# Kernel tuning notes

Measured on AMD Instinct MI355X. Metric: run time of the kernel, lower is better.

Reference implementation:

```python
import jax, jax.numpy as jnp
import numpy as np
from jax import lax

B = 256
INPUT_DIM = 65536
SEQ = 128
VOCAB = INPUT_DIM // SEQ  # 512
LATENT = 128
HIDS = (1024, 512, 256)   # encoder hidden dims (hidden_dims[:-1])
ENC_OUT = 128             # hidden_dims[-1]
GRU_H = 128               # decoder hidden_dim = hidden_dims[-1]
BN_EPS = 1e-5
LRELU_SLOPE = 0.01


def setup_inputs() -> dict:
    key = jax.random.key(0)
    ks = iter(jax.random.split(key, 40))
    def w(shape, scale=0.02):
        return (jax.random.normal(next(ks), shape, dtype=jnp.float32) * scale)
    d = {}
    d['x'] = jax.random.normal(next(ks), (B, INPUT_DIM), dtype=jnp.float32)
    d['eps'] = jax.random.normal(next(ks), (B, LATENT), dtype=jnp.float32)
    dims = (INPUT_DIM,) + HIDS
    # encoder Linear+BN stacks
    for i in range(3):
        d[f'W{i}'] = w((dims[i + 1], dims[i]))
        d[f'b{i}'] = w((dims[i + 1],))
        d[f'g{i}'] = jnp.ones((dims[i + 1],), jnp.float32)
        d[f'be{i}'] = jnp.zeros((dims[i + 1],), jnp.float32)
    d['Wout'] = w((ENC_OUT, HIDS[-1]))
    d['bout'] = w((ENC_OUT,))
    d['Wmu'] = w((LATENT, ENC_OUT)); d['bmu'] = w((LATENT,))
    d['Wlv'] = w((LATENT, ENC_OUT)); d['blv'] = w((LATENT,))
    # GRU (num_layers=1), PyTorch gate order r,z,n
    d['Wih'] = w((3 * GRU_H, LATENT)); d['bih'] = w((3 * GRU_H,))
    d['Whh'] = w((3 * GRU_H, GRU_H)); d['bhh'] = w((3 * GRU_H,))
    d['Wfc'] = w((VOCAB, GRU_H)); d['bfc'] = w((VOCAB,))
    return d


def _bn(h, g, b):
    m = jnp.mean(h, axis=0)
    v = jnp.var(h, axis=0)
    return (h - m) * lax.rsqrt(v + BN_EPS) * g + b


def _lrelu(h):
    return jnp.where(h > 0, h, LRELU_SLOPE * h)


def reference(x, eps, W0, b0, g0, be0, W1, b1, g1, be1, W2, b2, g2, be2,
              Wout, bout, Wmu, bmu, Wlv, blv, Wih, bih, Whh, bhh, Wfc, bfc):
    # ---- encode ----
    h = x
    for W, b, g, be in ((W0, b0, g0, be0), (W1, b1, g1, be1), (W2, b2, g2, be2)):
        h = _lrelu(_bn(h @ W.T + b, g, be))
    h = h @ Wout.T + bout
    h1 = jax.nn.relu(h)
    mu = h1 @ Wmu.T + bmu
    logvar = h1 @ Wlv.T + blv
    # ---- reparameterize ----
    z = mu + eps * jnp.exp(0.5 * logvar)
    # ---- greedy decode: GRU step + argmax + one-hot, seq_length times ----
    # GRU input is the constant z each step -> precompute input projection once
    xp = z @ Wih.T + bih                       # [B, 3H]
    xr, xz, xn = jnp.split(xp, 3, axis=1)
    h0 = jnp.zeros((x.shape[0], GRU_H), x.dtype)

    def step(hid, _):
        hp = hid @ Whh.T + bhh
        hr, hz, hn = jnp.split(hp, 3, axis=1)
        r = jax.nn.sigmoid(xr + hr)
        zg = jax.nn.sigmoid(xz + hz)
        n = jnp.tanh(xn + r * hn)
        h2 = (1.0 - zg) * n + zg * hid
        logits = h2 @ Wfc.T + bfc              # [B, V]
        oh = jax.nn.one_hot(jnp.argmax(logits, axis=1), VOCAB, dtype=logits.dtype)
        return h2, oh

    _, outs = lax.scan(step, h0, None, length=SEQ)  # [S, B, V]
    out = jnp.transpose(outs, (1, 0, 2))            # [B, S, V]
    return out, mu, logvar
```

## Files before the change

kernel.cpp:

```cpp
#include <hip/hip_runtime.h>

#define DI __device__ __forceinline__

typedef __attribute__((ext_vector_type(8))) short s16x8;
typedef __attribute__((ext_vector_type(4))) float f32x4;

DI f32x4 mfma16(s16x8 a, s16x8 b, f32x4 c) {
  return __builtin_amdgcn_mfma_f32_16x16x32_bf16(a, b, c, 0, 0, 0);
}

DI unsigned short f2bf(float f) {
  unsigned int u = __builtin_bit_cast(unsigned int, f);
  u += 0x7fffu + ((u >> 16) & 1u);
  return (unsigned short)(u >> 16);
}
DI float bf2f(unsigned short h) {
  unsigned int u = ((unsigned int)h) << 16;
  return __builtin_bit_cast(float, u);
}
DI void split2(float f, unsigned short &hi, unsigned short &lo) {
  hi = f2bf(f);
  lo = f2bf(f - bf2f(hi));
}

DI unsigned int cvtpk(float a, float b) {
  unsigned int r;
  asm("v_cvt_pk_bf16_f32 %0, %1, %2" : "=v"(r) : "v"(a), "v"(b));
  return r;
}
DI float fromlo(unsigned int u) { return __builtin_bit_cast(float, u << 16); }
DI float fromhi(unsigned int u) { return __builtin_bit_cast(float, u & 0xffff0000u); }

DI void write_pair8(unsigned short* hp, unsigned short* lp, float4 a, float4 b) {
  unsigned int h01 = cvtpk(a.x, a.y), h23 = cvtpk(a.z, a.w);
  unsigned int h45 = cvtpk(b.x, b.y), h67 = cvtpk(b.z, b.w);
  unsigned int l01 = cvtpk(a.x - fromlo(h01), a.y - fromhi(h01));
  unsigned int l23 = cvtpk(a.z - fromlo(h23), a.w - fromhi(h23));
  unsigned int l45 = cvtpk(b.x - fromlo(h45), b.y - fromhi(h45));
  unsigned int l67 = cvtpk(b.z - fromlo(h67), b.w - fromhi(h67));
  uint4 H4; H4.x = h01; H4.y = h23; H4.z = h45; H4.w = h67;
  uint4 L4; L4.x = l01; L4.y = l23; L4.z = l45; L4.w = l67;
  *(uint4*)hp = H4;
  *(uint4*)lp = L4;
}

DI float fsig(float x)  { return __builtin_amdgcn_rcpf(1.f + __expf(-x)); }
DI float ftanhf(float x){ return 1.f - 2.f * __builtin_amdgcn_rcpf(1.f + __expf(2.f * x)); }

template<int M, int N, int K, int KS, bool SWZ>
__global__ __launch_bounds__(256, 2) void k_gemm(const float* __restrict__ A,
                                                 const float* __restrict__ Bw,
                                                 float* __restrict__ P) {
  constexpr int MT = M / 128, NT = N / 128;
  constexpr int KC = K / KS;
  constexpr int ITERS = KC / 32;
  int bid = blockIdx.x;
  int kidx, mt, nt;
  if (SWZ) {
    int xcd = bid & 7, s = bid >> 3;
    kidx = xcd + 8 * (s >> 4);
    int mn = s & 15; mt = mn >> 3; nt = mn & 7;
  } else {
    kidx = bid / (MT * NT);
    int mn = bid % (MT * NT);
    mt = mn / NT; nt = mn % NT;
  }
  int tid = threadIdx.x;
  int w = tid >> 6, lane = tid & 63, q = lane >> 4, l15 = lane & 15;
  int wm = w >> 1, wn = w & 1;

  __shared__ unsigned short Ah[2][4][128][8], Al[2][4][128][8];
  __shared__ unsigned short Bh[2][4][128][8], Bl[2][4][128][8];

  int srow = tid >> 1;
  int skb  = (tid & 1) * 16;
  const float* Abase = A  + (size_t)(mt * 128 + srow) * K + (size_t)kidx * KC;
  const float* Bbase = Bw + (size_t)(nt * 128 + srow) * K + (size_t)kidx * KC;

  float4 ra[4], rb[4];
  auto loadit = [&](int it) {
    const float* pa = Abase + it * 32 + skb;
    const float* pb = Bbase + it * 32 + skb;
#pragma unroll
    for (int i = 0; i < 4; i++) {
      ra[i] = *(const float4*)(pa + 4 * i);
      rb[i] = *(const float4*)(pb + 4 * i);
    }
  };
  auto stage = [&](int pb) {
    int qq0 = skb >> 3;
    write_pair8(&Ah[pb][qq0][srow][0],     &Al[pb][qq0][srow][0],     ra[0], ra[1]);
    write_pair8(&Ah[pb][qq0 + 1][srow][0], &Al[pb][qq0 + 1][srow][0], ra[2], ra[3]);
    write_pair8(&Bh[pb][qq0][srow][0],     &Bl[pb][qq0][srow][0],     rb[0], rb[1]);
    write_pair8(&Bh[pb][qq0 + 1][srow][0], &Bl[pb][qq0 + 1][srow][0], rb[2], rb[3]);
  };

  f32x4 acc[4][4];
#pragma unroll
  for (int i = 0; i < 4; i++)
#pragma unroll
    for (int j = 0; j < 4; j++) acc[i][j] = (f32x4){0.f, 0.f, 0.f, 0.f};

  loadit(0);
  stage(0);
  loadit(1);

  for (int it = 0; it < ITERS; ++it) {
    __syncthreads();
    if (it + 1 < ITERS) stage((it + 1) & 1);
    if (it + 2 < ITERS) loadit(it + 2);
    int pr = it & 1;

    s16x8 afh[4], afl[4], bfh[4], bfl[4];
#pragma unroll
    for (int t = 0; t < 4; t++) {
      int m = wm * 64 + 16 * t + l15;
      afh[t] = *(const s16x8*)&Ah[pr][q][m][0];
      afl[t] = *(const s16x8*)&Al[pr][q][m][0];
      int n = wn * 64 + 16 * t + l15;
      bfh[t] = *(const s16x8*)&Bh[pr][q][n][0];
      bfl[t] = *(const s16x8*)&Bl[pr][q][n][0];
    }
#pragma unroll
    for (int ti = 0; ti < 4; ti++)
#pragma unroll
      for (int tj = 0; tj < 4; tj++)
        acc[ti][tj] = mfma16(afh[ti], bfh[tj], acc[ti][tj]);
#pragma unroll
    for (int ti = 0; ti < 4; ti++)
#pragma unroll
      for (int tj = 0; tj < 4; tj++)
        acc[ti][tj] = mfma16(afl[ti], bfh[tj], acc[ti][tj]);
#pragma unroll
    for (int ti = 0; ti < 4; ti++)
#pragma unroll
      for (int tj = 0; tj < 4; tj++)
        acc[ti][tj] = mfma16(afh[ti], bfl[tj], acc[ti][tj]);
  }
#pragma unroll
  for (int ti = 0; ti < 4; ti++)
#pragma unroll
    for (int tj = 0; tj < 4; tj++)
#pragma unroll
      for (int r = 0; r < 4; r++) {
        int row = mt * 128 + wm * 64 + 16 * ti + 4 * q + r;
        int col = nt * 128 + wn * 64 + 16 * tj + l15;
        P[((size_t)kidx * M + row) * N + col] = acc[ti][tj][r];
      }
}

template<int KS>
__global__ __launch_bounds__(256) void k_red(const float* __restrict__ P,
                                             float* __restrict__ O) {
  int idx = blockIdx.x * 256 + threadIdx.x;
  float s = 0.f;
#pragma unroll
  for (int kk = 0; kk < KS; kk++) s += P[(size_t)kk * 262144 + idx];
  O[idx] = s;
}

template<int KS, int N>
__global__ __launch_bounds__(256) void k_bn(const float* __restrict__ P,
                                            const float* __restrict__ g,
                                            const float* __restrict__ be,
                                            float* __restrict__ a) {
  int tid = threadIdx.x;
  int c = tid & 15, bg = tid >> 4;
  int col = blockIdx.x * 16 + c;
  __shared__ float hbuf[256][16];
  __shared__ float sbuf[16][16], s2buf[16][16];
  __shared__ float msc[16], msh[16];
  float s = 0.f, s2 = 0.f;
  for (int b = bg * 16; b < bg * 16 + 16; b++) {
    float h = 0.f;
#pragma unroll
    for (int kk = 0; kk < KS; kk++) h += P[((size_t)kk * 256 + b) * N + col];
    hbuf[b][c] = h;
    s += h; s2 += h * h;
  }
  sbuf[bg][c] = s; s2buf[bg][c] = s2;
  __syncthreads();
  if (bg == 0) {
    float ts = 0.f, ts2 = 0.f;
#pragma unroll
    for (int i = 0; i < 16; i++) { ts += sbuf[i][c]; ts2 += s2buf[i][c]; }
    float m = ts * (1.f / 256.f);
    float v = ts2 * (1.f / 256.f) - m * m;
    float rs = rsqrtf(v + 1e-5f);
    float sc = g[col] * rs;
    msc[c] = sc;
    msh[c] = be[col] - m * sc;
  }
  __syncthreads();
  float sc = msc[c], sh = msh[c];
  for (int b = bg * 16; b < bg * 16 + 16; b++) {
    float v = hbuf[b][c] * sc + sh;
    a[(size_t)b * N + col] = v > 0.f ? v : 0.01f * v;
  }
}

__global__ __launch_bounds__(128) void k_head(const float* __restrict__ P3,
    const float* __restrict__ bout,
    const float* __restrict__ Wmu, const float* __restrict__ bmu,
    const float* __restrict__ Wlv, const float* __restrict__ blv,
    const float* __restrict__ Wih, const float* __restrict__ bih,
    const float* __restrict__ eps,
    float* __restrict__ out_mu, float* __restrict__ out_lv,
    float* __restrict__ xp) {
  int b = blockIdx.x, j = threadIdx.x;
  __shared__ float es[128], zs[128];
  float e = P3[(size_t)b * 128 + j] + P3[(size_t)(256 + b) * 128 + j] + bout[j];
  es[j] = e > 0.f ? e : 0.f;
  __syncthreads();
  float mu = bmu[j], lv = blv[j];
  for (int k = 0; k < 128; k++) {
    mu += es[k] * Wmu[j * 128 + k];
    lv += es[k] * Wlv[j * 128 + k];
  }
  out_mu[b * 128 + j] = mu;
  out_lv[b * 128 + j] = lv;
  float z = mu + eps[b * 128 + j] * expf(0.5f * lv);
  zs[j] = z;
  __syncthreads();
  for (int gi = 0; gi < 3; gi++) {
    int row = gi * 128 + j;
    float s = bih[row];
    for (int k = 0; k < 128; k++) s += zs[k] * Wih[row * 128 + k];
    xp[(size_t)b * 384 + row] = s;
  }
}

__global__ __launch_bounds__(512, 2) void k_gru(const float* __restrict__ Whh,
    const float* __restrict__ bhh, const float* __restrict__ xp,
    float* __restrict__ H) {
  int b0 = blockIdx.x * 16;
  int tid = threadIdx.x;
  int w = tid >> 6, lane = tid & 63, q = lane >> 4, l15 = lane & 15;
  __shared__ unsigned short h2hi[2][16][136], h2lo[2][16][136];
  __shared__ float hstage[9][16][132];
  (void)lane;

  int rb3[3];
  rb3[0] = 16 * w;
  rb3[1] = 128 + 16 * w;
  rb3[2] = 256 + 16 * w;

  s16x8 wfh[3][4], wfl[3][4];
#pragma unroll
  for (int t = 0; t < 3; t++)
#pragma unroll
    for (int kt = 0; kt < 4; kt++) {
      const float* p = Whh + (size_t)(rb3[t] + l15) * 128 + kt * 32 + q * 8;
      s16x8 hi, lo;
#pragma unroll
      for (int j = 0; j < 8; j++) {
        unsigned short h, l; split2(p[j], h, l);
        hi[j] = (short)h; lo[j] = (short)l;
      }
      wfh[t][kt] = hi; wfl[t][kt] = lo;
    }

  int gb = b0 + l15;
  int k0 = 16 * w + 4 * q;
  float xr_[4], xz_[4], xn_[4], bhn_[4], hprev[4];
#pragma unroll
  for (int r = 0; r < 4; r++) {
    int kk = k0 + r;
    xr_[r] = xp[(size_t)gb * 384 + kk] + bhh[kk];
    xz_[r] = xp[(size_t)gb * 384 + 128 + kk] + bhh[128 + kk];
    xn_[r] = xp[(size_t)gb * 384 + 256 + kk];
    bhn_[r] = bhh[256 + kk];
    hprev[r] = 0.f;
  }

  for (int i = tid; i < 16 * 136; i += 512) {
    (&h2hi[0][0][0])[i] = 0;
    (&h2lo[0][0][0])[i] = 0;
  }
  __syncthreads();

  int hrow = tid >> 5, hcol = (tid & 31) * 4;
  int sl = 0;

  for (int s = 0; s < 128; s++) {
    int p = s & 1;
    s16x8 bhf[4], blf[4];
#pragma unroll
    for (int kt = 0; kt < 4; kt++) {
      bhf[kt] = *(const s16x8*)&h2hi[p][l15][kt * 32 + q * 8];
      blf[kt] = *(const s16x8*)&h2lo[p][l15][kt * 32 + q * 8];
    }
    if ((s & 7) == 0 && s) {
      int fb = s - 8;
#pragma unroll
      for (int ss = 0; ss < 8; ss++) {
        int t9 = sl + 1 + ss;
        int fsl = t9 >= 9 ? t9 - 9 : t9;
        float4 v = *(const float4*)&hstage[fsl][hrow][hcol];
        *(float4*)(H + ((size_t)(b0 + hrow) * 128 + fb + ss) * 128 + hcol) = v;
      }
    }

    f32x4 accm[3], accc[3];
#pragma unroll
    for (int t = 0; t < 3; t++) {
      accm[t] = (f32x4){0.f, 0.f, 0.f, 0.f};
      accc[t] = (f32x4){0.f, 0.f, 0.f, 0.f};
    }
#pragma unroll
    for (int kt = 0; kt < 4; kt++) {
#pragma unroll
      for (int t = 0; t < 3; t++) accm[t] = mfma16(wfh[t][kt], bhf[kt], accm[t]);
#pragma unroll
      for (int t = 0; t < 3; t++) accc[t] = mfma16(wfl[t][kt], bhf[kt], accc[t]);
#pragma unroll
      for (int t = 0; t < 3; t++) accc[t] = mfma16(wfh[t][kt], blf[kt], accc[t]);
    }

    float hv[4];
#pragma unroll
    for (int r = 0; r < 4; r++) {
      float hr = accm[0][r] + accc[0][r];
      float hz = accm[1][r] + accc[1][r];
      float hn = accm[2][r] + accc[2][r];
      float rg = fsig(xr_[r] + hr);
      float zg = fsig(xz_[r] + hz);
      float ng = ftanhf(fmaf(rg, hn + bhn_[r], xn_[r]));
      float h2 = fmaf(zg, hprev[r] - ng, ng);
      hprev[r] = h2;
      hv[r] = h2;
    }
    unsigned int h01 = cvtpk(hv[0], hv[1]), h23 = cvtpk(hv[2], hv[3]);
    unsigned int l01 = cvtpk(hv[0] - fromlo(h01), hv[1] - fromhi(h01));
    unsigned int l23 = cvtpk(hv[2] - fromlo(h23), hv[3] - fromhi(h23));
    *(float4*)&hstage[sl][l15][k0] = make_float4(hv[0], hv[1], hv[2], hv[3]);
    uint2 hh; hh.x = h01; hh.y = h23;
    uint2 ll; ll.x = l01; ll.y = l23;
    *(uint2*)&h2hi[p ^ 1][l15][k0] = hh;
    *(uint2*)&h2lo[p ^ 1][l15][k0] = ll;
    sl = (sl == 8) ? 0 : sl + 1;
    __syncthreads();
  }
#pragma unroll
  for (int ss = 0; ss < 8; ss++) {
    int fb = 120 + ss;
    int fsl = fb % 9;
    float4 v = *(const float4*)&hstage[fsl][hrow][hcol];
    *(float4*)(H + ((size_t)(b0 + hrow) * 128 + fb) * 128 + hcol) = v;
  }
}

__global__ __launch_bounds__(256, 2) void k_fc(const float* __restrict__ H,
    const float* __restrict__ Wfc, const float* __restrict__ bfc,
    float* __restrict__ out) {
  int rows0 = blockIdx.x * 64;
  int tid = threadIdx.x;
  int w = tid >> 6, lane = tid & 63, q = lane >> 4, l15 = lane & 15;
  __shared__ unsigned short Ah[4][4][64][8], Al[4][4][64][8];
  __shared__ unsigned short Bh[4][4][32][8], Bl[4][4][32][8];
  __shared__ int argbuf[64];
  (void)lane;

  {
    int row = tid >> 2, kb = (tid & 3) * 32;
    const float* p = H + (size_t)(rows0 + row) * 128 + kb;
    int kt = kb >> 5;
    float4 v[8];
#pragma unroll
    for (int i = 0; i < 8; i++) v[i] = *(const float4*)(p + 4 * i);
#pragma unroll
    for (int j = 0; j < 4; j++)
      write_pair8(&Ah[kt][j][row][0], &Al[kt][j][row][0], v[2 * j], v[2 * j + 1]);
  }
  __syncthreads();

  s16x8 afh[4], afl[4];
#pragma unroll
  for (int kt = 0; kt < 4; kt++) {
    afh[kt] = *(const s16x8*)&Ah[kt][q][16 * w + l15][0];
    afl[kt] = *(const s16x8*)&Al[kt][q][16 * w + l15][0];
  }

  float best[4]; int bidx[4];
#pragma unroll
  for (int r = 0; r < 4; r++) { best[r] = -3.4e38f; bidx[r] = 0; }

  for (int c = 0; c < 16; c++) {
    {
      int n = tid >> 3, kb = (tid & 7) * 16;
      const float* p = Wfc + (size_t)(c * 32 + n) * 128 + kb;
      int kt = kb >> 5, qq0 = (kb >> 3) & 3;
      float4 v0 = *(const float4*)(p);
      float4 v1 = *(const float4*)(p + 4);
      float4 v2 = *(const float4*)(p + 8);
      float4 v3 = *(const float4*)(p + 12);
      write_pair8(&Bh[kt][qq0][n][0],     &Bl[kt][qq0][n][0],     v0, v1);
      write_pair8(&Bh[kt][qq0 + 1][n][0], &Bl[kt][qq0 + 1][n][0], v2, v3);
    }
    __syncthreads();
    f32x4 acc[2];
    acc[0] = (f32x4){0.f, 0.f, 0.f, 0.f};
    acc[1] = (f32x4){0.f, 0.f, 0.f, 0.f};
    s16x8 bh[2][4], bl[2][4];
#pragma unroll
    for (int nt = 0; nt < 2; nt++)
#pragma unroll
      for (int kt = 0; kt < 4; kt++) {
        bh[nt][kt] = *(const s16x8*)&Bh[kt][q][nt * 16 + l15][0];
        bl[nt][kt] = *(const s16x8*)&Bl[kt][q][nt * 16 + l15][0];
      }
#pragma unroll
    for (int kt = 0; kt < 4; kt++)
#pragma unroll
      for (int nt = 0; nt < 2; nt++) {
        acc[nt] = mfma16(afh[kt], bh[nt][kt], acc[nt]);
        acc[nt] = mfma16(afl[kt], bh[nt][kt], acc[nt]);
        acc[nt] = mfma16(afh[kt], bl[nt][kt], acc[nt]);
      }
#pragma unroll
    for (int nt = 0; nt < 2; nt++)
#pragma unroll
      for (int r = 0; r < 4; r++) {
        int col = c * 32 + nt * 16 + l15;
        float v = acc[nt][r] + bfc[col];
        if (v > best[r]) { best[r] = v; bidx[r] = col; }
      }
    __syncthreads();
  }

#pragma unroll
  for (int r = 0; r < 4; r++) {
    float bv = best[r]; int bi = bidx[r];
    for (int off = 8; off >= 1; off >>= 1) {
      float ov = __shfl_xor(bv, off, 64);
      int oi = __shfl_xor(bi, off, 64);
      if (ov > bv || (ov == bv && oi < bi)) { bv = ov; bi = oi; }
    }
    if (l15 == 0) argbuf[16 * w + 4 * q + r] = bi;
  }
  __syncthreads();

  int row = tid >> 2, cb = (tid & 3) * 128;
  int am = argbuf[row];
  float* op = out + (size_t)(rows0 + row) * 512 + cb;
#pragma unroll
  for (int i = 0; i < 32; i++) {
    float4 v = {0.f, 0.f, 0.f, 0.f};
    int base = cb + 4 * i;
    if (am >= base && am < base + 4) ((float*)&v)[am - base] = 1.0f;
    *(float4*)(op + 4 * i) = v;
  }
}

extern "C" void kernel_launch(void* const* d_in, const int* in_sizes, int n_in,
                              void* d_out, int out_size, void* d_ws, size_t ws_size,
                              hipStream_t stream) {
  const float* x    = (const float*)d_in[0];
  const float* eps  = (const float*)d_in[1];
  const float* W0   = (const float*)d_in[2];
  const float* g0   = (const float*)d_in[4];
  const float* be0  = (const float*)d_in[5];
  const float* W1   = (const float*)d_in[6];
  const float* g1   = (const float*)d_in[8];
  const float* be1  = (const float*)d_in[9];
  const float* W2   = (const float*)d_in[10];
  const float* g2   = (const float*)d_in[12];
  const float* be2  = (const float*)d_in[13];
  const float* Wout = (const float*)d_in[14];
  const float* bout = (const float*)d_in[15];
  const float* Wmu  = (const float*)d_in[16];
  const float* bmu  = (const float*)d_in[17];
  const float* Wlv  = (const float*)d_in[18];
  const float* blv  = (const float*)d_in[19];
  const float* Wih  = (const float*)d_in[20];
  const float* bih  = (const float*)d_in[21];
  const float* Whh  = (const float*)d_in[22];
  const float* bhh  = (const float*)d_in[23];
  const float* Wfc  = (const float*)d_in[24];
  const float* bfc  = (const float*)d_in[25];

  float* out    = (float*)d_out;
  float* mu_out = out + 16777216;
  float* lv_out = out + 16777216 + 32768;

  const bool big = ws_size >= 75900000ull;
  const int KS0 = big ? 64 : 16;

  float* ws  = (float*)d_ws;
  float* P0  = ws;
  float* O0  = ws + (size_t)262144 * KS0;
  float* a1  = O0 + 262144;
  float* P1  = a1 + 262144;
  float* a2  = P1 + 1048576;
  float* P2  = a2 + 131072;
  float* a3  = P2 + 262144;
  float* P3  = a3 + 65536;
  float* xp  = P3 + 65536;
  float* Hst = ws;

  if (big) {
    hipLaunchKernelGGL((k_gemm<256,1024,65536,64,true>), dim3(1024), dim3(256), 0, stream, x, W0, P0);
    hipLaunchKernelGGL((k_red<64>),                      dim3(1024), dim3(256), 0, stream, P0, O0);
  } else {
    hipLaunchKernelGGL((k_gemm<256,1024,65536,16,true>), dim3(256),  dim3(256), 0, stream, x, W0, P0);
    hipLaunchKernelGGL((k_red<16>),                      dim3(1024), dim3(256), 0, stream, P0, O0);
  }
  hipLaunchKernelGGL((k_bn<1,1024>),                   dim3(64),  dim3(256), 0, stream, O0, g0, be0, a1);
  hipLaunchKernelGGL((k_gemm<256,512,1024,8,false>),   dim3(64),  dim3(256), 0, stream, a1, W1, P1);
  hipLaunchKernelGGL((k_bn<8,512>),                    dim3(32),  dim3(256), 0, stream, P1, g1, be1, a2);
  hipLaunchKernelGGL((k_gemm<256,256,512,4,false>),    dim3(16),  dim3(256), 0, stream, a2, W2, P2);
  hipLaunchKernelGGL((k_bn<4,256>),                    dim3(16),  dim3(256), 0, stream, P2, g2, be2, a3);
  hipLaunchKernelGGL((k_gemm<256,128,256,2,false>),    dim3(4),   dim3(256), 0, stream, a3, Wout, P3);
  hipLaunchKernelGGL(k_head, dim3(256), dim3(128), 0, stream, P3, bout, Wmu, bmu, Wlv, blv, Wih, bih, eps, mu_out, lv_out, xp);
  hipLaunchKernelGGL(k_gru,  dim3(16),  dim3(512), 0, stream, Whh, bhh, xp, Hst);
  hipLaunchKernelGGL(k_fc,   dim3(512), dim3(256), 0, stream, Hst, Wfc, bfc, out);
}
```

Before: 785.5 us.

## Prefetch LDS fragments across barriers and use LDS-only barriers with MFMA priority

In the split-K GEMM, the next stage's LDS fragments are now read right after the barrier, so the loop runs one barrier per iteration with fragment reads overlapping global loads. __syncthreads is replaced by an lgkmcnt-only wait plus s_barrier, so outstanding global loads no longer stall at barriers. MFMA blocks are wrapped in s_setprio. The FC kernel register-prefetches the next Wfc chunk while the current one is computed. These changes aim to hide memory latency, at the cost of extra registers and careful ordering of the LDS hazards.

```diff
diff --git a/kernel.cpp b/kernel.cpp
--- a/kernel.cpp
+++ b/kernel.cpp
@@ -7,6 +7,11 @@
 
 DI f32x4 mfma16(s16x8 a, s16x8 b, f32x4 c) {
   return __builtin_amdgcn_mfma_f32_16x16x32_bf16(a, b, c, 0, 0, 0);
+}
+
+DI void lds_barrier() {
+  asm volatile("s_waitcnt lgkmcnt(0)" ::: "memory");
+  __builtin_amdgcn_s_barrier();
 }
 
 DI unsigned short f2bf(float f) {
@@ -54,6 +59,7 @@
   constexpr int MT = M / 128, NT = N / 128;
   constexpr int KC = K / KS;
   constexpr int ITERS = KC / 32;
+  static_assert(ITERS >= 2, "pipeline needs ITERS>=2");
   int bid = blockIdx.x;
   int kidx, mt, nt;
   if (SWZ) {
@@ -95,23 +101,8 @@
     write_pair8(&Bh[pb][qq0 + 1][srow][0], &Bl[pb][qq0 + 1][srow][0], rb[2], rb[3]);
   };
 
-  f32x4 acc[4][4];
-#pragma unroll
-  for (int i = 0; i < 4; i++)
-#pragma unroll
-    for (int j = 0; j < 4; j++) acc[i][j] = (f32x4){0.f, 0.f, 0.f, 0.f};
-
-  loadit(0);
-  stage(0);
-  loadit(1);
-
-  for (int it = 0; it < ITERS; ++it) {
-    __syncthreads();
-    if (it + 1 < ITERS) stage((it + 1) & 1);
-    if (it + 2 < ITERS) loadit(it + 2);
-    int pr = it & 1;
-
-    s16x8 afh[4], afl[4], bfh[4], bfl[4];
+  s16x8 afh[4], afl[4], bfh[4], bfl[4];
+  auto readfrags = [&](int pr) {
 #pragma unroll
     for (int t = 0; t < 4; t++) {
       int m = wm * 64 + 16 * t + l15;
@@ -121,6 +112,26 @@
       bfh[t] = *(const s16x8*)&Bh[pr][q][n][0];
       bfl[t] = *(const s16x8*)&Bl[pr][q][n][0];
     }
+  };
+
+  f32x4 acc[4][4];
+#pragma unroll
+  for (int i = 0; i < 4; i++)
+#pragma unroll
+    for (int j = 0; j < 4; j++) acc[i][j] = (f32x4){0.f, 0.f, 0.f, 0.f};
+
+  loadit(0);
+  stage(0);
+  loadit(1);
+  lds_barrier();
+  readfrags(0);
+
+  for (int it = 0; it < ITERS; ++it) {
+    int pr = it & 1;
+    if (it + 1 < ITERS) stage(pr ^ 1);
+    if (it + 2 < ITERS) loadit(it + 2);
+
+    __builtin_amdgcn_s_setprio(1);
 #pragma unroll
     for (int ti = 0; ti < 4; ti++)
 #pragma unroll
@@ -136,7 +147,12 @@
 #pragma unroll
       for (int tj = 0; tj < 4; tj++)
         acc[ti][tj] = mfma16(afh[ti], bfl[tj], acc[ti][tj]);
-  }
+    __builtin_amdgcn_s_setprio(0);
+
+    lds_barrier();
+    if (it + 1 < ITERS) readfrags(pr ^ 1);
+  }
+
 #pragma unroll
   for (int ti = 0; ti < 4; ti++)
 #pragma unroll
@@ -307,6 +323,7 @@
       accm[t] = (f32x4){0.f, 0.f, 0.f, 0.f};
       accc[t] = (f32x4){0.f, 0.f, 0.f, 0.f};
     }
+    __builtin_amdgcn_s_setprio(1);
 #pragma unroll
     for (int kt = 0; kt < 4; kt++) {
 #pragma unroll
@@ -316,6 +333,7 @@
 #pragma unroll
       for (int t = 0; t < 3; t++) accc[t] = mfma16(wfh[t][kt], blf[kt], accc[t]);
     }
+    __builtin_amdgcn_s_setprio(0);
 
     float hv[4];
 #pragma unroll
@@ -339,7 +357,7 @@
     *(uint2*)&h2hi[p ^ 1][l15][k0] = hh;
     *(uint2*)&h2lo[p ^ 1][l15][k0] = ll;
     sl = (sl == 8) ? 0 : sl + 1;
-    __syncthreads();
+    lds_barrier();
   }
 #pragma unroll
   for (int ss = 0; ss < 8; ss++) {
@@ -372,7 +390,7 @@
     for (int j = 0; j < 4; j++)
       write_pair8(&Ah[kt][j][row][0], &Al[kt][j][row][0], v[2 * j], v[2 * j + 1]);
   }
-  __syncthreads();
+  lds_barrier();
 
   s16x8 afh[4], afl[4];
 #pragma unroll
@@ -385,37 +403,46 @@
 #pragma unroll
   for (int r = 0; r < 4; r++) { best[r] = -3.4e38f; bidx[r] = 0; }
 
+  int n = tid >> 3, kb = (tid & 7) * 16;
+  int kt = kb >> 5, qq0 = (kb >> 3) & 3;
+  float4 cur0, cur1, cur2, cur3;
+  {
+    const float* p = Wfc + (size_t)n * 128 + kb;
+    cur0 = *(const float4*)(p);
+    cur1 = *(const float4*)(p + 4);
+    cur2 = *(const float4*)(p + 8);
+    cur3 = *(const float4*)(p + 12);
+  }
+
   for (int c = 0; c < 16; c++) {
-    {
-      int n = tid >> 3, kb = (tid & 7) * 16;
-      const float* p = Wfc + (size_t)(c * 32 + n) * 128 + kb;
-      int kt = kb >> 5, qq0 = (kb >> 3) & 3;
-      float4 v0 = *(const float4*)(p);
-      float4 v1 = *(const float4*)(p + 4);
-      float4 v2 = *(const float4*)(p + 8);
-      float4 v3 = *(const float4*)(p + 12);
-      write_pair8(&Bh[kt][qq0][n][0],     &Bl[kt][qq0][n][0],     v0, v1);
-      write_pair8(&Bh[kt][qq0 + 1][n][0], &Bl[kt][qq0 + 1][n][0], v2, v3);
-    }
-    __syncthreads();
+    write_pair8(&Bh[kt][qq0][n][0],     &Bl[kt][qq0][n][0],     cur0, cur1);
+    write_pair8(&Bh[kt][qq0 + 1][n][0], &Bl[kt][qq0 + 1][n][0], cur2, cur3);
+    if (c + 1 < 16) {
+      const float* p = Wfc + (size_t)((c + 1) * 32 + n) * 128 + kb;
+      cur0 = *(const float4*)(p);
+      cur1 = *(const float4*)(p + 4);
+      cur2 = *(const float4*)(p + 8);
+      cur3 = *(const float4*)(p + 12);
+    }
+    lds_barrier();
     f32x4 acc[2];
     acc[0] = (f32x4){0.f, 0.f, 0.f, 0.f};
     acc[1] = (f32x4){0.f, 0.f, 0.f, 0.f};
     s16x8 bh[2][4], bl[2][4];
 #pragma unroll
-    for (int nt = 0; nt < 2; nt++)
-#pragma unroll
-      for (int kt = 0; kt < 4; kt++) {
-        bh[nt][kt] = *(const s16x8*)&Bh[kt][q][nt * 16 + l15][0];
-        bl[nt][kt] = *(const s16x8*)&Bl[kt][q][nt * 16 + l15][0];
+    for (int kk = 0; kk < 4; kk++)
+#pragma unroll
+      for (int nt = 0; nt < 2; nt++) {
+        bh[nt][kk] = *(const s16x8*)&Bh[kk][q][nt * 16 + l15][0];
+        bl[nt][kk] = *(const s16x8*)&Bl[kk][q][nt * 16 + l15][0];
       }
 #pragma unroll
-    for (int kt = 0; kt < 4; kt++)
+    for (int kk = 0; kk < 4; kk++)
 #pragma unroll
       for (int nt = 0; nt < 2; nt++) {
-        acc[nt] = mfma16(afh[kt], bh[nt][kt], acc[nt]);
-        acc[nt] = mfma16(afl[kt], bh[nt][kt], acc[nt]);
-        acc[nt] = mfma16(afh[kt], bl[nt][kt], acc[nt]);
+        acc[nt] = mfma16(afh[kk], bh[nt][kk], acc[nt]);
+        acc[nt] = mfma16(afl[kk], bh[nt][kk], acc[nt]);
+        acc[nt] = mfma16(afh[kk], bl[nt][kk], acc[nt]);
       }
 #pragma unroll
     for (int nt = 0; nt < 2; nt++)
@@ -425,7 +452,7 @@
         float v = acc[nt][r] + bfc[col];
         if (v > best[r]) { best[r] = v; bidx[r] = col; }
       }
-    __syncthreads();
+    lds_barrier();
   }
 
 #pragma unroll
```

After: 791.0 us. About the same (+0.7%).
